# Performance work log

Hardware: AMD Instinct MI355X
Metric: run time of the kernel (lower is better)

## Reference

```python
import jax, jax.numpy as jnp
import numpy as np

N = 100000   # nodes
E = 1600000  # edges (before self-loops)
F_IN = 128
H = 64
G = 512      # graphs in batch


def _add_self_loops(edge_index, n):
    loop = jnp.arange(n, dtype=edge_index.dtype)
    src = jnp.concatenate([edge_index[0], loop])
    dst = jnp.concatenate([edge_index[1], loop])
    return src, dst


def _gcn_norm(src, dst, n):
    # PyG GCNConv: deg over targets with self-loops, norm = d^-1/2[src]*d^-1/2[dst]
    deg = jax.ops.segment_sum(jnp.ones_like(dst, dtype=jnp.float32), dst, num_segments=n)
    dinv = jnp.where(deg > 0, jax.lax.rsqrt(deg), 0.0)
    return dinv[src] * dinv[dst]


def _gcn_conv(x, src, dst, norm, W, b):
    xw = x @ W                                # [N, H]
    msg = xw[src] * norm[:, None]             # [E+N, H] gather + scale
    out = jax.ops.segment_sum(msg, dst, num_segments=x.shape[0])
    return out + b


def setup_inputs() -> dict:
    key = jax.random.key(0)
    ks = jax.random.split(key, 9)
    x = jax.random.normal(ks[0], (N, F_IN), dtype=jnp.float32)
    edge_index = jax.random.randint(ks[1], (2, E), 0, N, dtype=jnp.int32)
    batch = jnp.sort(jax.random.randint(ks[2], (N,), 0, G, dtype=jnp.int32))
    s1 = 1.0 / np.sqrt(F_IN)
    s2 = 1.0 / np.sqrt(H)
    W1 = jax.random.uniform(ks[3], (F_IN, H), jnp.float32, -s1, s1)
    b1 = jnp.zeros((H,), jnp.float32)
    W2 = jax.random.uniform(ks[4], (H, H), jnp.float32, -s2, s2)
    b2 = jnp.zeros((H,), jnp.float32)
    Wl = jax.random.uniform(ks[5], (H, 1), jnp.float32, -s2, s2)
    bl = jnp.zeros((1,), jnp.float32)
    return {"x": x, "edge_index": edge_index, "batch": batch,
            "W1": W1, "b1": b1, "W2": W2, "b2": b2, "Wl": Wl, "bl": bl}


def reference(x, edge_index, batch, W1, b1, W2, b2, Wl, bl):
    n = x.shape[0]
    src, dst = _add_self_loops(edge_index, n)
    norm = _gcn_norm(src, dst, n)
    h = jax.nn.relu(_gcn_conv(x, src, dst, norm, W1, b1))
    h = jax.nn.relu(_gcn_conv(h, src, dst, norm, W2, b2))
    # global mean pool over graphs
    sums = jax.ops.segment_sum(h, batch, num_segments=G)          # [G, H]
    cnt = jax.ops.segment_sum(jnp.ones((n,), jnp.float32), batch, num_segments=G)
    pooled = sums / jnp.maximum(cnt, 1.0)[:, None]
    return jax.nn.sigmoid(pooled @ Wl + bl)                        # [G, 1]
```

## Files before the change

### kernel.cpp

```cpp
#include <hip/hip_runtime.h>
#include <hip/hip_bf16.h>
#include <cmath>

#define F_IN 128
#define HDIM 64
#define NPB 256
#define NB1 1024

typedef __attribute__((ext_vector_type(8))) short bf16x8;
typedef __attribute__((ext_vector_type(4))) float f32x4;

__device__ __forceinline__ float bf2f(unsigned short u) {
    union { unsigned int i; float f; } v; v.i = ((unsigned int)u) << 16; return v.f;
}
__device__ __forceinline__ unsigned short f2bf(float f) {
    __hip_bfloat16 h = __float2bfloat16(f);
    union { __hip_bfloat16 h; unsigned short u; } c; c.h = h; return c.u;
}


__launch_bounds__(256)
__global__ void p0_count(const int* __restrict__ dst, int* __restrict__ blk_cnt,
                         int E, int nbuk, int chunk) {
    __shared__ int hist[512];
    int tid = threadIdx.x;
    for (int i = tid; i < nbuk; i += 256) hist[i] = 0;
    __syncthreads();
    int lo = blockIdx.x * chunk;
    int hi = min(E, lo + chunk);
    for (int e = lo + tid; e < hi; e += 256)
        atomicAdd(&hist[dst[e] >> 8], 1);
    __syncthreads();
    for (int i = tid; i < nbuk; i += 256)
        blk_cnt[i * NB1 + blockIdx.x] = hist[i];
}

__launch_bounds__(256)
__global__ void p_scan_blocks(int* __restrict__ blk_cnt, int* __restrict__ bucket_cnt) {
    __shared__ int sd[256];
    int b = blockIdx.x, tid = threadIdx.x;
    int4* row = (int4*)(blk_cnt + (size_t)b * NB1);
    int4 v = row[tid];
    int s0 = v.x, s1 = s0 + v.y, s2 = s1 + v.z, s3 = s2 + v.w;
    sd[tid] = s3;
    __syncthreads();
    for (int off = 1; off < 256; off <<= 1) {
        int a = (tid >= off) ? sd[tid - off] : 0;
        __syncthreads();
        sd[tid] += a;
        __syncthreads();
    }
    int base = sd[tid] - s3;
    int4 o;
    o.x = base; o.y = base + s0; o.z = base + s1; o.w = base + s2;
    row[tid] = o;
    if (tid == 255) bucket_cnt[b] = sd[255];
}

__global__ void p0_scan(const int* __restrict__ cnt, int* __restrict__ base, int nbuk) {
    __shared__ int sd[512];
    int tid = threadIdx.x;
    int v = (tid < nbuk) ? cnt[tid] : 0;
    sd[tid] = v;
    __syncthreads();
    for (int off = 1; off < 512; off <<= 1) {
        int a = (tid >= off) ? sd[tid - off] : 0;
        __syncthreads();
        sd[tid] += a;
        __syncthreads();
    }
    if (tid < nbuk) base[tid] = sd[tid] - v;
    if (tid == nbuk - 1) base[nbuk] = sd[tid];
}

__launch_bounds__(256)
__global__ void p1_place(const int* __restrict__ src, const int* __restrict__ dst,
                         const int* __restrict__ blk_cnt, const int* __restrict__ bucket_base,
                         int* __restrict__ pairs, int E, int nbuk, int chunk) {
    __shared__ int cur[512];
    int tid = threadIdx.x;
    for (int i = tid; i < nbuk; i += 256)
        cur[i] = bucket_base[i] + blk_cnt[i * NB1 + blockIdx.x];
    __syncthreads();
    int lo = blockIdx.x * chunk;
    int hi = min(E, lo + chunk);
    for (int e = lo + tid; e < hi; e += 256) {
        int d = dst[e];
        int pos = atomicAdd(&cur[d >> 8], 1);
        pairs[pos] = (src[e] << 8) | (d & 255);
    }
}

__launch_bounds__(256)
__global__ void p2_csr(const int* __restrict__ pairs, const int* __restrict__ base,
                       int* __restrict__ row_start, int* __restrict__ deg,
                       float* __restrict__ dinv, int* __restrict__ col, int n) {
    __shared__ int dl[256];
    __shared__ int sc[256];
    __shared__ int cur[256];
    int b = blockIdx.x, tid = threadIdx.x;
    int nlo = b << 8;
    int eb = base[b], ee = base[b + 1];
    dl[tid] = 0;
    __syncthreads();
    for (int e = eb + tid; e < ee; e += 256)
        atomicAdd(&dl[pairs[e] & 255], 1);
    __syncthreads();
    int d0 = dl[tid];
    sc[tid] = d0;
    __syncthreads();
    for (int off = 1; off < 256; off <<= 1) {
        int a = (tid >= off) ? sc[tid - off] : 0;
        __syncthreads();
        sc[tid] += a;
        __syncthreads();
    }
    int excl = sc[tid] - d0;
    int node = nlo + tid;
    if (node < n) {
        row_start[node] = eb + excl;
        deg[node] = d0;
        dinv[node] = rsqrtf((float)(d0 + 1));
    }
    cur[tid] = eb + excl;
    __syncthreads();
    for (int e = eb + tid; e < ee; e += 256) {
        unsigned int v = (unsigned int)pairs[e];
        int pos = atomicAdd(&cur[v & 255], 1);
        col[pos] = (int)(v >> 8);
    }
}


__global__ void graph_bounds(const int* __restrict__ batch, int* __restrict__ gstart,
                             int n, int G) {
    int g = blockIdx.x * blockDim.x + threadIdx.x;
    if (g > G) return;
    int lo = 0, hi = n;
    while (lo < hi) {
        int mid = (lo + hi) >> 1;
        if (batch[mid] < g) lo = mid + 1; else hi = mid;
    }
    gstart[g] = lo;
}


template <int K>
__launch_bounds__(256)
__global__ void matmul_mfma(const float* __restrict__ X, const float* __restrict__ W,
                            const float* __restrict__ dinv, unsigned short* __restrict__ out,
                            int n) {
    constexpr int KS  = K / 32;
    constexpr int LDX = K + 8;
    __shared__ unsigned short Xs[64 * LDX];
    __shared__ unsigned short Wss[K * HDIM];

    int tid = threadIdx.x;
    int rowbase = blockIdx.x * 64;

    {
        const float4* W4 = (const float4*)W;
        for (int i = tid; i < K * HDIM / 4; i += 256) {
            float4 v = W4[i];
            ushort4 u = { f2bf(v.x), f2bf(v.y), f2bf(v.z), f2bf(v.w) };
            *(ushort4*)(Wss + i * 4) = u;
        }
    }
    {
        const float4* X4 = (const float4*)X;
        for (int i = tid; i < 64 * K / 4; i += 256) {
            int r = i / (K / 4), k4 = i % (K / 4);
            ushort4 u = { 0, 0, 0, 0 };
            int gr = rowbase + r;
            if (gr < n) {
                float4 v = X4[(size_t)gr * (K / 4) + k4];
                u.x = f2bf(v.x); u.y = f2bf(v.y); u.z = f2bf(v.z); u.w = f2bf(v.w);
            }
            *(ushort4*)(Xs + r * LDX + k4 * 4) = u;
        }
    }
    __syncthreads();

    int wave = tid >> 6, lane = tid & 63;
    int q = lane >> 4, nn = lane & 15;

    bf16x8 bfrag[KS][4];
#pragma unroll
    for (int s = 0; s < KS; ++s)
#pragma unroll
        for (int c = 0; c < 4; ++c) {
            short tmp[8];
#pragma unroll
            for (int j = 0; j < 8; ++j)
                tmp[j] = (short)Wss[(s * 32 + q * 8 + j) * HDIM + c * 16 + nn];
            bfrag[s][c] = *(bf16x8*)tmp;
        }

    f32x4 acc[4] = {{0,0,0,0},{0,0,0,0},{0,0,0,0},{0,0,0,0}};
    int mrow = wave * 16 + nn;
#pragma unroll
    for (int s = 0; s < KS; ++s) {
        bf16x8 af = *(const bf16x8*)(Xs + mrow * LDX + s * 32 + q * 8);
#pragma unroll
        for (int c = 0; c < 4; ++c)
            acc[c] = __builtin_amdgcn_mfma_f32_16x16x32_bf16(af, bfrag[s][c], acc[c], 0, 0, 0);
    }

#pragma unroll
    for (int r = 0; r < 4; ++r) {
        int row = rowbase + wave * 16 + q * 4 + r;
        if (row >= n) continue;
        float dv = dinv[row];
#pragma unroll
        for (int c = 0; c < 4; ++c)
            out[(size_t)row * HDIM + c * 16 + nn] = f2bf(acc[c][r] * dv);
    }
}


__global__ void csr_gather(const int* __restrict__ col, const int* __restrict__ row_start,
                           const int* __restrict__ deg, const float* __restrict__ dinv,
                           const ushort4* __restrict__ xws, const float* __restrict__ bias,
                           float4* __restrict__ out, int n) {
    int t = blockIdx.x * blockDim.x + threadIdx.x;
    int node = t >> 4;
    if (node >= n) return;
    int lane = t & 15;
    int s = row_start[node];
    int end = s + deg[node];

    ushort4 sv = xws[(size_t)node * 16 + lane];
    float4 acc = { bf2f(sv.x), bf2f(sv.y), bf2f(sv.z), bf2f(sv.w) };
    int e = s;
    for (; e + 4 <= end; e += 4) {
        int c0 = col[e], c1 = col[e + 1], c2 = col[e + 2], c3 = col[e + 3];
        ushort4 v0 = xws[(size_t)c0 * 16 + lane];
        ushort4 v1 = xws[(size_t)c1 * 16 + lane];
        ushort4 v2 = xws[(size_t)c2 * 16 + lane];
        ushort4 v3 = xws[(size_t)c3 * 16 + lane];
        acc.x += (bf2f(v0.x) + bf2f(v1.x)) + (bf2f(v2.x) + bf2f(v3.x));
        acc.y += (bf2f(v0.y) + bf2f(v1.y)) + (bf2f(v2.y) + bf2f(v3.y));
        acc.z += (bf2f(v0.z) + bf2f(v1.z)) + (bf2f(v2.z) + bf2f(v3.z));
        acc.w += (bf2f(v0.w) + bf2f(v1.w)) + (bf2f(v2.w) + bf2f(v3.w));
    }
    for (; e < end; ++e) {
        int c = col[e];
        ushort4 v = xws[(size_t)c * 16 + lane];
        acc.x += bf2f(v.x); acc.y += bf2f(v.y); acc.z += bf2f(v.z); acc.w += bf2f(v.w);
    }
    float dv = dinv[node];
    const float4 b4 = *(const float4*)(bias + lane * 4);
    float4 o;
    o.x = fmaxf(fmaf(acc.x, dv, b4.x), 0.0f);
    o.y = fmaxf(fmaf(acc.y, dv, b4.y), 0.0f);
    o.z = fmaxf(fmaf(acc.z, dv, b4.z), 0.0f);
    o.w = fmaxf(fmaf(acc.w, dv, b4.w), 0.0f);
    out[(size_t)node * 16 + lane] = o;
}


__launch_bounds__(256)
__global__ void pool_head(const float* __restrict__ h, const int* __restrict__ gstart,
                          const float* __restrict__ Wl, const float* __restrict__ bl,
                          float* __restrict__ out, int G) {
    int g = blockIdx.x;
    int s = gstart[g], e = gstart[g + 1];
    int f  = threadIdx.x & 63;
    int rg = threadIdx.x >> 6;
    float acc = 0.0f;
    for (int i = s + rg; i < e; i += 4)
        acc += h[(size_t)i * HDIM + f];
    __shared__ float red[4][HDIM];
    red[rg][f] = acc;
    __syncthreads();
    if (rg == 0) {
        float v = (red[0][f] + red[1][f]) + (red[2][f] + red[3][f]);
        float c = fmaxf((float)(e - s), 1.0f);
        v = v * Wl[f] * (1.0f / c);
#pragma unroll
        for (int off = 32; off; off >>= 1) v += __shfl_down(v, off, 64);
        if (f == 0) out[g] = 1.0f / (1.0f + expf(-(v + bl[0])));
    }
}


extern "C" void kernel_launch(void* const* d_in, const int* in_sizes, int n_in,
                              void* d_out, int out_size, void* d_ws, size_t ws_size,
                              hipStream_t stream) {
    const float* x   = (const float*)d_in[0];
    const int* ei    = (const int*)d_in[1];
    const int* batch = (const int*)d_in[2];
    const float* W1  = (const float*)d_in[3];
    const float* b1  = (const float*)d_in[4];
    const float* W2  = (const float*)d_in[5];
    const float* b2  = (const float*)d_in[6];
    const float* Wl  = (const float*)d_in[7];
    const float* bl  = (const float*)d_in[8];
    float* out = (float*)d_out;

    const int n = in_sizes[0] / F_IN;
    const int E = in_sizes[1] / 2;
    const int G = out_size;

    const int* srcp = ei;
    const int* dstp = ei + E;

    int nbuk = (n + NPB - 1) / NPB;

    char* wsb = (char*)d_ws;
    auto alloc = [&](size_t bytes) { char* p = wsb; wsb += (bytes + 255) & ~(size_t)255; return p; };
    int*   deg        = (int*)alloc((size_t)n * 4);
    int*   row_start  = (int*)alloc((size_t)n * 4);
    float* dinv       = (float*)alloc((size_t)n * 4);
    int*   bucket_cnt = (int*)alloc(512 * 4);
    int*   bucket_base= (int*)alloc(513 * 4);
    int*   blk_cnt    = (int*)alloc((size_t)nbuk * NB1 * 4);
    int*   pairs      = (int*)alloc((size_t)E * 4);
    int*   colx       = (int*)alloc((size_t)E * 4);
    unsigned short* xwsb = (unsigned short*)alloc((size_t)n * HDIM * 2);
    float* bufB       = (float*)alloc((size_t)n * HDIM * 4);
    int*   gstart     = (int*)alloc(((size_t)G + 1) * 4);

    const int TB = 256;
    int gN16 = (n * 16 + TB - 1) / TB;
    int gMM  = (n + 63) / 64;
    int chunk = (E + NB1 - 1) / NB1;

    p0_count<<<NB1, TB, 0, stream>>>(dstp, blk_cnt, E, nbuk, chunk);
    p_scan_blocks<<<nbuk, TB, 0, stream>>>(blk_cnt, bucket_cnt);
    p0_scan<<<1, 512, 0, stream>>>(bucket_cnt, bucket_base, nbuk);
    p1_place<<<NB1, TB, 0, stream>>>(srcp, dstp, blk_cnt, bucket_base, pairs, E, nbuk, chunk);
    p2_csr<<<nbuk, TB, 0, stream>>>(pairs, bucket_base, row_start, deg, dinv, colx, n);
    graph_bounds<<<(G + 1 + TB - 1) / TB, TB, 0, stream>>>(batch, gstart, n, G);

    matmul_mfma<F_IN><<<gMM, 256, 0, stream>>>(x, W1, dinv, xwsb, n);
    csr_gather<<<gN16, TB, 0, stream>>>(colx, row_start, deg, dinv,
                                        (const ushort4*)xwsb, b1, (float4*)bufB, n);

    matmul_mfma<HDIM><<<gMM, 256, 0, stream>>>(bufB, W2, dinv, xwsb, n);
    csr_gather<<<gN16, TB, 0, stream>>>(colx, row_start, deg, dinv,
                                        (const ushort4*)xwsb, b2, (float4*)bufB, n);

    pool_head<<<G, 256, 0, stream>>>(bufB, gstart, Wl, bl, out, G);
}
```

Measured before the change: 280.0 us.

## Degree-sort nodes per bucket, widen gather to 8 lanes, store layer-1 output in bf16

p2_csr now also builds, per 256-node bucket, a permutation of nodes sorted by in-degree (capped at 63), so lanes grouped together in the gather do similar amounts of work. The gather kernel uses 8 lanes per node with 16-byte bf16x8 loads instead of 16 lanes with 8-byte loads. The first layer writes its output as bf16, and a new bf16-input matmul reads it for layer 2, halving that intermediate traffic. The costs are extra bf16 rounding of the hidden activations, scattered node order in the output writes, and a serial 64-bin prefix sum per block.

```diff
diff --git a/kernel.cpp b/kernel.cpp
--- a/kernel.cpp
+++ b/kernel.cpp
@@ -94,14 +94,18 @@
 __launch_bounds__(256)
 __global__ void p2_csr(const int* __restrict__ pairs, const int* __restrict__ base,
                        int* __restrict__ row_start, int* __restrict__ deg,
-                       float* __restrict__ dinv, int* __restrict__ col, int n) {
+                       float* __restrict__ dinv, int* __restrict__ col,
+                       int* __restrict__ order, int n) {
     __shared__ int dl[256];
     __shared__ int sc[256];
     __shared__ int cur[256];
+    __shared__ int h64[64];
+    __shared__ int s64[64];
     int b = blockIdx.x, tid = threadIdx.x;
     int nlo = b << 8;
     int eb = base[b], ee = base[b + 1];
     dl[tid] = 0;
+    if (tid < 64) h64[tid] = 0;
     __syncthreads();
     for (int e = eb + tid; e < ee; e += 256)
         atomicAdd(&dl[pairs[e] & 255], 1);
@@ -123,11 +127,19 @@
         dinv[node] = rsqrtf((float)(d0 + 1));
     }
     cur[tid] = eb + excl;
-    __syncthreads();
+    int bin = min(d0, 63);
+    atomicAdd(&h64[bin], 1);
+    __syncthreads();
+    if (tid == 0) { int run = 0; for (int i = 0; i < 64; ++i) { s64[i] = run; run += h64[i]; } }
+    __syncthreads();
+    if (tid < 64) h64[tid] = 0;
+    __syncthreads();
+    int pos = s64[bin] + atomicAdd(&h64[bin], 1);
+    order[nlo + pos] = (node < n) ? node : 0x7fffffff;
     for (int e = eb + tid; e < ee; e += 256) {
         unsigned int v = (unsigned int)pairs[e];
-        int pos = atomicAdd(&cur[v & 255], 1);
-        col[pos] = (int)(v >> 8);
+        int p = atomicAdd(&cur[v & 255], 1);
+        col[p] = (int)(v >> 8);
     }
 }
 
@@ -218,44 +230,131 @@
 }
 
 
-__global__ void csr_gather(const int* __restrict__ col, const int* __restrict__ row_start,
-                           const int* __restrict__ deg, const float* __restrict__ dinv,
-                           const ushort4* __restrict__ xws, const float* __restrict__ bias,
-                           float4* __restrict__ out, int n) {
-    int t = blockIdx.x * blockDim.x + threadIdx.x;
-    int node = t >> 4;
+__launch_bounds__(256)
+__global__ void matmul_mfma_b16(const unsigned short* __restrict__ X, const float* __restrict__ W,
+                                const float* __restrict__ dinv, unsigned short* __restrict__ out,
+                                int n) {
+    constexpr int K = 64, KS = 2, LDX = K + 8;
+    __shared__ unsigned short Xs[64 * LDX];
+    __shared__ unsigned short Wss[K * HDIM];
+
+    int tid = threadIdx.x;
+    int rowbase = blockIdx.x * 64;
+
+    {
+        const float4* W4 = (const float4*)W;
+        for (int i = tid; i < K * HDIM / 4; i += 256) {
+            float4 v = W4[i];
+            ushort4 u = { f2bf(v.x), f2bf(v.y), f2bf(v.z), f2bf(v.w) };
+            *(ushort4*)(Wss + i * 4) = u;
+        }
+    }
+    {
+        for (int i = tid; i < 64 * 8; i += 256) {
+            int r = i >> 3, c = i & 7;
+            int gr = rowbase + r;
+            bf16x8 u;
+            if (gr < n) u = ((const bf16x8*)X)[(size_t)gr * 8 + c];
+            else { short z[8] = {0,0,0,0,0,0,0,0}; u = *(bf16x8*)z; }
+            *(bf16x8*)(Xs + r * LDX + c * 8) = u;
+        }
+    }
+    __syncthreads();
+
+    int wave = tid >> 6, lane = tid & 63;
+    int q = lane >> 4, nn = lane & 15;
+
+    bf16x8 bfrag[KS][4];
+#pragma unroll
+    for (int s = 0; s < KS; ++s)
+#pragma unroll
+        for (int c = 0; c < 4; ++c) {
+            short tmp[8];
+#pragma unroll
+            for (int j = 0; j < 8; ++j)
+                tmp[j] = (short)Wss[(s * 32 + q * 8 + j) * HDIM + c * 16 + nn];
+            bfrag[s][c] = *(bf16x8*)tmp;
+        }
+
+    f32x4 acc[4] = {{0,0,0,0},{0,0,0,0},{0,0,0,0},{0,0,0,0}};
+    int mrow = wave * 16 + nn;
+#pragma unroll
+    for (int s = 0; s < KS; ++s) {
+        bf16x8 af = *(const bf16x8*)(Xs + mrow * LDX + s * 32 + q * 8);
+#pragma unroll
+        for (int c = 0; c < 4; ++c)
+            acc[c] = __builtin_amdgcn_mfma_f32_16x16x32_bf16(af, bfrag[s][c], acc[c], 0, 0, 0);
+    }
+
+#pragma unroll
+    for (int r = 0; r < 4; ++r) {
+        int row = rowbase + wave * 16 + q * 4 + r;
+        if (row >= n) continue;
+        float dv = dinv[row];
+#pragma unroll
+        for (int c = 0; c < 4; ++c)
+            out[(size_t)row * HDIM + c * 16 + nn] = f2bf(acc[c][r] * dv);
+    }
+}
+
+
+template <bool OUT_BF16>
+__launch_bounds__(256)
+__global__ void csr_gather8(const int* __restrict__ order, const int* __restrict__ col,
+                            const int* __restrict__ rs, const int* __restrict__ deg,
+                            const float* __restrict__ dinv, const bf16x8* __restrict__ xws,
+                            const float* __restrict__ bias, void* __restrict__ outv,
+                            int nslots, int n) {
+    int t = blockIdx.x * 256 + threadIdx.x;
+    int slot = t >> 3;
+    if (slot >= nslots) return;
+    int L = t & 7;
+    int node = order[slot];
     if (node >= n) return;
-    int lane = t & 15;
-    int s = row_start[node];
+    int s = rs[node];
     int end = s + deg[node];
 
-    ushort4 sv = xws[(size_t)node * 16 + lane];
-    float4 acc = { bf2f(sv.x), bf2f(sv.y), bf2f(sv.z), bf2f(sv.w) };
+    bf16x8 sv = xws[(size_t)node * 8 + L];
+    float a[8];
+#pragma unroll
+    for (int j = 0; j < 8; ++j) a[j] = bf2f((unsigned short)sv[j]);
+
     int e = s;
     for (; e + 4 <= end; e += 4) {
         int c0 = col[e], c1 = col[e + 1], c2 = col[e + 2], c3 = col[e + 3];
-        ushort4 v0 = xws[(size_t)c0 * 16 + lane];
-        ushort4 v1 = xws[(size_t)c1 * 16 + lane];
-        ushort4 v2 = xws[(size_t)c2 * 16 + lane];
-        ushort4 v3 = xws[(size_t)c3 * 16 + lane];
-        acc.x += (bf2f(v0.x) + bf2f(v1.x)) + (bf2f(v2.x) + bf2f(v3.x));
-        acc.y += (bf2f(v0.y) + bf2f(v1.y)) + (bf2f(v2.y) + bf2f(v3.y));
-        acc.z += (bf2f(v0.z) + bf2f(v1.z)) + (bf2f(v2.z) + bf2f(v3.z));
-        acc.w += (bf2f(v0.w) + bf2f(v1.w)) + (bf2f(v2.w) + bf2f(v3.w));
+        bf16x8 v0 = xws[(size_t)c0 * 8 + L];
+        bf16x8 v1 = xws[(size_t)c1 * 8 + L];
+        bf16x8 v2 = xws[(size_t)c2 * 8 + L];
+        bf16x8 v3 = xws[(size_t)c3 * 8 + L];
+#pragma unroll
+        for (int j = 0; j < 8; ++j)
+            a[j] += (bf2f((unsigned short)v0[j]) + bf2f((unsigned short)v1[j])) +
+                    (bf2f((unsigned short)v2[j]) + bf2f((unsigned short)v3[j]));
     }
     for (; e < end; ++e) {
         int c = col[e];
-        ushort4 v = xws[(size_t)c * 16 + lane];
-        acc.x += bf2f(v.x); acc.y += bf2f(v.y); acc.z += bf2f(v.z); acc.w += bf2f(v.w);
-    }
+        bf16x8 v = xws[(size_t)c * 8 + L];
+#pragma unroll
+        for (int j = 0; j < 8; ++j) a[j] += bf2f((unsigned short)v[j]);
+    }
+
     float dv = dinv[node];
-    const float4 b4 = *(const float4*)(bias + lane * 4);
-    float4 o;
-    o.x = fmaxf(fmaf(acc.x, dv, b4.x), 0.0f);
-    o.y = fmaxf(fmaf(acc.y, dv, b4.y), 0.0f);
-    o.z = fmaxf(fmaf(acc.z, dv, b4.z), 0.0f);
-    o.w = fmaxf(fmaf(acc.w, dv, b4.w), 0.0f);
-    out[(size_t)node * 16 + lane] = o;
+    int f0 = L * 8;
+    float r[8];
+#pragma unroll
+    for (int j = 0; j < 8; ++j)
+        r[j] = fmaxf(fmaf(a[j], dv, bias[f0 + j]), 0.0f);
+
+    if (OUT_BF16) {
+        bf16x8 o;
+#pragma unroll
+        for (int j = 0; j < 8; ++j) o[j] = (short)f2bf(r[j]);
+        ((bf16x8*)outv)[(size_t)node * 8 + L] = o;
+    } else {
+        float4* op = (float4*)outv + (size_t)node * 16 + L * 2;
+        op[0] = make_float4(r[0], r[1], r[2], r[3]);
+        op[1] = make_float4(r[4], r[5], r[6], r[7]);
+    }
 }
 
 
@@ -306,40 +405,43 @@
     const int* dstp = ei + E;
 
     int nbuk = (n + NPB - 1) / NPB;
+    int nslots = nbuk * NPB;
 
     char* wsb = (char*)d_ws;
     auto alloc = [&](size_t bytes) { char* p = wsb; wsb += (bytes + 255) & ~(size_t)255; return p; };
     int*   deg        = (int*)alloc((size_t)n * 4);
     int*   row_start  = (int*)alloc((size_t)n * 4);
     float* dinv       = (float*)alloc((size_t)n * 4);
+    int*   order      = (int*)alloc((size_t)nslots * 4);
     int*   bucket_cnt = (int*)alloc(512 * 4);
     int*   bucket_base= (int*)alloc(513 * 4);
     int*   blk_cnt    = (int*)alloc((size_t)nbuk * NB1 * 4);
     int*   pairs      = (int*)alloc((size_t)E * 4);
     int*   colx       = (int*)alloc((size_t)E * 4);
     unsigned short* xwsb = (unsigned short*)alloc((size_t)n * HDIM * 2);
+    unsigned short* xh1  = (unsigned short*)alloc((size_t)n * HDIM * 2);
     float* bufB       = (float*)alloc((size_t)n * HDIM * 4);
     int*   gstart     = (int*)alloc(((size_t)G + 1) * 4);
 
     const int TB = 256;
-    int gN16 = (n * 16 + TB - 1) / TB;
     int gMM  = (n + 63) / 64;
     int chunk = (E + NB1 - 1) / NB1;
+    int gG8  = (nslots * 8 + TB - 1) / TB;
 
     p0_count<<<NB1, TB, 0, stream>>>(dstp, blk_cnt, E, nbuk, chunk);
     p_scan_blocks<<<nbuk, TB, 0, stream>>>(blk_cnt, bucket_cnt);
     p0_scan<<<1, 512, 0, stream>>>(bucket_cnt, bucket_base, nbuk);
     p1_place<<<NB1, TB, 0, stream>>>(srcp, dstp, blk_cnt, bucket_base, pairs, E, nbuk, chunk);
-    p2_csr<<<nbuk, TB, 0, stream>>>(pairs, bucket_base, row_start, deg, dinv, colx, n);
+    p2_csr<<<nbuk, TB, 0, stream>>>(pairs, bucket_base, row_start, deg, dinv, colx, order, n);
     graph_bounds<<<(G + 1 + TB - 1) / TB, TB, 0, stream>>>(batch, gstart, n, G);
 
     matmul_mfma<F_IN><<<gMM, 256, 0, stream>>>(x, W1, dinv, xwsb, n);
-    csr_gather<<<gN16, TB, 0, stream>>>(colx, row_start, deg, dinv,
-                                        (const ushort4*)xwsb, b1, (float4*)bufB, n);
-
-    matmul_mfma<HDIM><<<gMM, 256, 0, stream>>>(bufB, W2, dinv, xwsb, n);
-    csr_gather<<<gN16, TB, 0, stream>>>(colx, row_start, deg, dinv,
-                                        (const ushort4*)xwsb, b2, (float4*)bufB, n);
+    csr_gather8<true><<<gG8, TB, 0, stream>>>(order, colx, row_start, deg, dinv,
+                                              (const bf16x8*)xwsb, b1, xh1, nslots, n);
+
+    matmul_mfma_b16<<<gMM, 256, 0, stream>>>(xh1, W2, dinv, xwsb, n);
+    csr_gather8<false><<<gG8, TB, 0, stream>>>(order, colx, row_start, deg, dinv,
+                                               (const bf16x8*)xwsb, b2, bufB, nslots, n);
 
     pool_head<<<G, 256, 0, stream>>>(bufB, gstart, Wl, bl, out, G);
 }
```

After: 287.7 us. +2.8%, slower.
